# Optimization experiments

Measured on AMD Instinct MI355X. Metric: run time of the kernel, lower is better.

The kernel has to match this reference:

```python
import jax, jax.numpy as jnp
import numpy as np

N, E = 50000, 1_000_000
IN_F, OUT_F = 128, 64
NEG_SLOPE = 0.2


def setup_inputs() -> dict:
    key = jax.random.key(0)
    k1, k2, k3, k4, k5 = jax.random.split(key, 5)
    x = jax.random.normal(k1, (N, IN_F), dtype=jnp.float32)
    edge_index = jax.random.randint(k2, (2, E), 0, N, dtype=jnp.int64)
    # xavier_uniform with gain=1.414 (as in the torch init)
    gain = 1.414
    bW = gain * np.sqrt(6.0 / (IN_F + OUT_F))
    W = jax.random.uniform(k3, (IN_F, OUT_F), jnp.float32, -bW, bW)
    ba = gain * np.sqrt(6.0 / (OUT_F + 1))
    a_src = jax.random.uniform(k4, (OUT_F, 1), jnp.float32, -ba, ba)
    a_dst = jax.random.uniform(k5, (OUT_F, 1), jnp.float32, -ba, ba)
    return {"x": x, "edge_index": edge_index, "W": W, "a_src": a_src, "a_dst": a_dst}


def reference(x, edge_index, W, a_src, a_dst):
    n = x.shape[0]
    Wh = x @ W                                  # [N, F_out]
    src = edge_index[0]
    dst = edge_index[1]
    # per-edge attention logits: (Wh[src] . a_src) + (Wh[dst] . a_dst)
    s_src = Wh @ a_src[:, 0]                    # [N]
    s_dst = Wh @ a_dst[:, 0]                    # [N]
    e = jax.nn.leaky_relu(s_src[src] + s_dst[dst], negative_slope=NEG_SLOPE)  # [E]
    e = jnp.exp(e - jnp.max(e))                 # global-max stabilized exp (matches torch code)
    denom = jax.ops.segment_sum(e, dst, num_segments=n) + 1e-16  # [N]
    alpha = e / denom[dst]                      # [E]  (dropout p=0 -> identity)
    out = jax.ops.segment_sum(Wh[src] * alpha[:, None], dst, num_segments=n)  # [N, F_out]
    return jax.nn.elu(out)
```

## Files before the change

### kernel.cpp

```cpp
#include <hip/hip_runtime.h>
#include <hip/hip_bf16.h>
#include <math.h>

#define NN 50000
#define NE 1000000
#define FIN 128
#define FOUT 64
#define NEG 0.2f

#define NB     1024
#define DPB    50
#define NBUSED 1000
#define TS     4096
#define PADCAP 1280
#define TILE_BLKS 245
#define GEMM_BLKS 391

using short8  = __attribute__((ext_vector_type(8))) short;
using floatx4 = __attribute__((ext_vector_type(4))) float;

static __device__ __forceinline__ short f2bf(float f) {
    __hip_bfloat16 h = __float2bfloat16(f);
    return *(short*)&h;
}

__global__ __launch_bounds__(512) void k_front(
    const float* __restrict__ x, const float* __restrict__ W,
    const float* __restrict__ a_src, const float* __restrict__ a_dst,
    const int* __restrict__ ei,
    __hip_bfloat16* __restrict__ Whb, float* __restrict__ s_src,
    float* __restrict__ s_dst,
    int* __restrict__ bcur, unsigned* __restrict__ bdata2)
{
    __shared__ int cnt[NB];
    __shared__ int ofs[NB];
    __shared__ int cur[NB];
    __shared__ int gpos[NB];
    __shared__ unsigned srt[TS];
    __shared__ int wsum[8];

    const int tid  = threadIdx.x;
    const int lane = tid & 63;
    const int wv   = tid >> 6;

    if (blockIdx.x >= TILE_BLKS) {
        const int col  = lane & 15;
        const int quad = lane >> 4;
        const int strip = (blockIdx.x - TILE_BLKS) * 8 + wv;
        if (strip >= NN / 16) return;
        const int row0 = strip * 16;

        short8 bfr[4][4];
        #pragma unroll
        for (int kk = 0; kk < 4; ++kk) {
            #pragma unroll
            for (int nt = 0; nt < 4; ++nt) {
                const float* wp = W + (kk * 32 + quad * 8) * FOUT + nt * 16 + col;
                #pragma unroll
                for (int j = 0; j < 8; ++j)
                    bfr[kk][nt][j] = f2bf(wp[j * FOUT]);
            }
        }

        floatx4 acc[4] = {{0.f,0.f,0.f,0.f},{0.f,0.f,0.f,0.f},
                          {0.f,0.f,0.f,0.f},{0.f,0.f,0.f,0.f}};

        const float* xrow = x + (size_t)(row0 + col) * FIN + quad * 8;
        #pragma unroll
        for (int kk = 0; kk < 4; ++kk) {
            const float4 u0 = *(const float4*)(xrow + kk * 32);
            const float4 u1 = *(const float4*)(xrow + kk * 32 + 4);
            short8 af;
            af[0] = f2bf(u0.x); af[1] = f2bf(u0.y);
            af[2] = f2bf(u0.z); af[3] = f2bf(u0.w);
            af[4] = f2bf(u1.x); af[5] = f2bf(u1.y);
            af[6] = f2bf(u1.z); af[7] = f2bf(u1.w);
            #pragma unroll
            for (int nt = 0; nt < 4; ++nt)
                acc[nt] = __builtin_amdgcn_mfma_f32_16x16x32_bf16(
                    af, bfr[kk][nt], acc[nt], 0, 0, 0);
        }

        const float av0 = a_src[col], av1 = a_src[16 + col];
        const float av2 = a_src[32 + col], av3 = a_src[48 + col];
        const float bv0 = a_dst[col], bv1 = a_dst[16 + col];
        const float bv2 = a_dst[32 + col], bv3 = a_dst[48 + col];

        float ps[4], pd[4];
        #pragma unroll
        for (int reg = 0; reg < 4; ++reg) {
            ps[reg] = acc[0][reg] * av0 + acc[1][reg] * av1
                    + acc[2][reg] * av2 + acc[3][reg] * av3;
            pd[reg] = acc[0][reg] * bv0 + acc[1][reg] * bv1
                    + acc[2][reg] * bv2 + acc[3][reg] * bv3;
        }

        #pragma unroll
        for (int nt = 0; nt < 4; ++nt)
            #pragma unroll
            for (int reg = 0; reg < 4; ++reg)
                Whb[(size_t)(row0 + quad * 4 + reg) * FOUT + nt * 16 + col] =
                    __float2bfloat16(acc[nt][reg]);

        #pragma unroll
        for (int off = 1; off < 16; off <<= 1) {
            #pragma unroll
            for (int reg = 0; reg < 4; ++reg) {
                ps[reg] += __shfl_xor(ps[reg], off);
                pd[reg] += __shfl_xor(pd[reg], off);
            }
        }
        if (col == 0) {
            #pragma unroll
            for (int reg = 0; reg < 4; ++reg) {
                s_src[row0 + quad * 4 + reg] = ps[reg];
                s_dst[row0 + quad * 4 + reg] = pd[reg];
            }
        }
        return;
    }

    const int tile = blockIdx.x;
    const int base = tile * TS;
    const int tcnt = (NE - base < TS) ? (NE - base) : TS;

    cnt[tid] = 0; cnt[tid + 512] = 0;
    __syncthreads();

    unsigned pk[8];
    #pragma unroll
    for (int j = 0; j < 8; ++j) {
        const int i = j * 512 + tid;
        if (i < tcnt) {
            const int e = base + i;
            const unsigned s = (unsigned)__builtin_nontemporal_load(ei + e);
            const unsigned d = (unsigned)__builtin_nontemporal_load(ei + NE + e);
            pk[j] = (s << 16) | d;
            atomicAdd(&cnt[d / DPB], 1);
        } else pk[j] = 0xFFFFFFFFu;
    }
    __syncthreads();

    {
        const int i0 = tid * 2;
        const int v0 = cnt[i0], v1 = cnt[i0 + 1];
        const int s = v0 + v1;
        int inc = s;
        #pragma unroll
        for (int off = 1; off < 64; off <<= 1) {
            const int t = __shfl_up(inc, off);
            if (lane >= off) inc += t;
        }
        if (lane == 63) wsum[wv] = inc;
        __syncthreads();
        int wb = 0;
        #pragma unroll
        for (int w = 0; w < 7; ++w) if (w < wv) wb += wsum[w];
        const int excl = wb + inc - s;
        ofs[i0]     = excl;      ofs[i0 + 1] = excl + v0;
        cur[i0]     = excl;      cur[i0 + 1] = excl + v0;
        if (v0 > 0) gpos[i0]     = i0 * PADCAP + atomicAdd(&bcur[i0], v0);
        if (v1 > 0) gpos[i0 + 1] = (i0 + 1) * PADCAP + atomicAdd(&bcur[i0 + 1], v1);
    }
    __syncthreads();

    #pragma unroll
    for (int j = 0; j < 8; ++j) {
        if (pk[j] != 0xFFFFFFFFu) {
            const int b = (int)(pk[j] & 0xffffu) / DPB;
            const int pos = atomicAdd(&cur[b], 1);
            srt[pos] = pk[j];
        }
    }
    __syncthreads();

    for (int i = tid; i < tcnt; i += 512) {
        const unsigned p = srt[i];
        const int bb = (int)(p & 0xffffu) / DPB;
        const int dpos = gpos[bb] + (i - ofs[bb]);
        if (dpos < (bb + 1) * PADCAP) bdata2[dpos] = p;
    }
}

__global__ __launch_bounds__(512) void k_sortgather(
    const int* __restrict__ bcur, const unsigned* __restrict__ bdata2,
    const float* __restrict__ s_src, const float* __restrict__ s_dst,
    const __hip_bfloat16* __restrict__ Whb, float* __restrict__ out)
{
    __shared__ unsigned raw[PADCAP];
    __shared__ unsigned srt[PADCAP];
    __shared__ float evs[PADCAP];
    __shared__ float sdl[DPB];
    __shared__ int cnt[64];
    __shared__ int ofs2[65];
    __shared__ int cur[64];

    const int b = blockIdx.x;
    const int tid = threadIdx.x;
    const int lane = tid & 63;
    const int wv = tid >> 6;
    const int d0 = b * DPB;

    if (tid < 64) cnt[tid] = 0;
    if (tid < DPB) sdl[tid] = s_dst[d0 + tid];

    int tot = bcur[b];
    if (tot > PADCAP) tot = PADCAP;
    const unsigned* slab = bdata2 + (size_t)b * PADCAP;

    for (int i = tid; i < tot; i += 512) raw[i] = slab[i];
    __syncthreads();

    for (int i = tid; i < tot; i += 512)
        atomicAdd(&cnt[(int)(raw[i] & 0xffffu) - d0], 1);
    __syncthreads();

    if (tid < 64) {
        const int cc = (tid < DPB) ? cnt[tid] : 0;
        int in2 = cc;
        #pragma unroll
        for (int off = 1; off < 64; off <<= 1) {
            const int t = __shfl_up(in2, off);
            if (tid >= off) in2 += t;
        }
        ofs2[tid + 1] = in2;
        if (tid == 0) ofs2[0] = 0;
        cur[tid] = in2 - cc;
    }
    __syncthreads();

    for (int i = tid; i < tot; i += 512) {
        const unsigned p = raw[i];
        const int j = (int)(p & 0xffffu) - d0;
        const int pos = atomicAdd(&cur[j], 1);
        srt[pos] = p;
        float v = s_src[p >> 16] + sdl[j];
        v = (v > 0.f) ? v : NEG * v;
        evs[pos] = __expf(v);
    }
    __syncthreads();

    for (int j = wv; j < DPB; j += 8) {
        const int d = d0 + j;
        const int beg = ofs2[j];
        const int end = ofs2[j + 1];
        float acc = 0.f, den = 0.f;
        int i = beg;
        for (; i + 8 <= end; i += 8) {
            int ss[8]; float ee[8], w[8];
            #pragma unroll
            for (int k = 0; k < 8; ++k) {
                ss[k] = (int)(srt[i + k] >> 16);
                ee[k] = evs[i + k];
            }
            #pragma unroll
            for (int k = 0; k < 8; ++k)
                w[k] = __bfloat162float(Whb[(size_t)ss[k] * FOUT + lane]);
            #pragma unroll
            for (int k = 0; k < 8; ++k) {
                acc = fmaf(ee[k], w[k], acc);
                den += ee[k];
            }
        }
        for (; i < end; ++i) {
            const int s0 = (int)(srt[i] >> 16);
            const float e0 = evs[i];
            acc = fmaf(e0, __bfloat162float(Whb[(size_t)s0 * FOUT + lane]), acc);
            den += e0;
        }
        const float r = acc / (den + 1e-16f);
        out[(size_t)d * FOUT + lane] = (r > 0.f) ? r : expm1f(r);
    }
}

extern "C" void kernel_launch(void* const* d_in, const int* in_sizes, int n_in,
                              void* d_out, int out_size, void* d_ws, size_t ws_size,
                              hipStream_t stream)
{
    const float* x     = (const float*)d_in[0];
    const int*   ei    = (const int*)d_in[1];
    const float* W     = (const float*)d_in[2];
    const float* a_src = (const float*)d_in[3];
    const float* a_dst = (const float*)d_in[4];
    float* out = (float*)d_out;

    float* ws    = (float*)d_ws;
    __hip_bfloat16* Whb = (__hip_bfloat16*)ws;
    float* s_src = ws + (size_t)NN * FOUT / 2;
    float* s_dst = s_src + NN;
    int*   bcur  = (int*)(s_dst + NN);
    unsigned* bdata2 = (unsigned*)(bcur + NB);

    hipMemsetAsync(bcur, 0, NB * sizeof(int), stream);
    k_front<<<TILE_BLKS + GEMM_BLKS, 512, 0, stream>>>(
        x, W, a_src, a_dst, ei, Whb, s_src, s_dst, bcur, bdata2);
    k_sortgather<<<NBUSED, 512, 0, stream>>>(bcur, bdata2, s_src, s_dst,
                                             Whb, out);
}
```

Baseline: 129.9 us.

## Replace per-destination counting sort with LDS atomic accumulation in gather kernel

The gather kernel no longer counting-sorts edges by destination within each bucket. Each wave takes an even contiguous share of the bucket's edges and atomically adds exp-weighted Wh rows into a shared-memory accumulator, with denominators also summed by atomics. This drops two barriers, the histogram and the scan, and balances load across waves regardless of in-degree skew. In exchange it adds LDS float atomics per edge and lane, which can contend when edges share a destination, and makes the summation order nondeterministic.

After: 453.1 us. 249% more time.

```diff
diff --git a/kernel.cpp b/kernel.cpp
--- a/kernel.cpp
+++ b/kernel.cpp
@@ -182,18 +182,16 @@
     }
 }
 
-__global__ __launch_bounds__(512) void k_sortgather(
+__global__ __launch_bounds__(512) void k_accgather(
     const int* __restrict__ bcur, const unsigned* __restrict__ bdata2,
     const float* __restrict__ s_src, const float* __restrict__ s_dst,
     const __hip_bfloat16* __restrict__ Whb, float* __restrict__ out)
 {
     __shared__ unsigned raw[PADCAP];
-    __shared__ unsigned srt[PADCAP];
     __shared__ float evs[PADCAP];
+    __shared__ float accum[DPB * FOUT];
+    __shared__ float den[DPB];
     __shared__ float sdl[DPB];
-    __shared__ int cnt[64];
-    __shared__ int ofs2[65];
-    __shared__ int cur[64];
 
     const int b = blockIdx.x;
     const int tid = threadIdx.x;
@@ -201,75 +199,55 @@
     const int wv = tid >> 6;
     const int d0 = b * DPB;
 
-    if (tid < 64) cnt[tid] = 0;
-    if (tid < DPB) sdl[tid] = s_dst[d0 + tid];
+    for (int i = tid; i < DPB * FOUT; i += 512) accum[i] = 0.f;
+    if (tid < DPB) { den[tid] = 0.f; sdl[tid] = s_dst[d0 + tid]; }
 
     int tot = bcur[b];
     if (tot > PADCAP) tot = PADCAP;
     const unsigned* slab = bdata2 + (size_t)b * PADCAP;
-
     for (int i = tid; i < tot; i += 512) raw[i] = slab[i];
-    __syncthreads();
-
-    for (int i = tid; i < tot; i += 512)
-        atomicAdd(&cnt[(int)(raw[i] & 0xffffu) - d0], 1);
-    __syncthreads();
-
-    if (tid < 64) {
-        const int cc = (tid < DPB) ? cnt[tid] : 0;
-        int in2 = cc;
-        #pragma unroll
-        for (int off = 1; off < 64; off <<= 1) {
-            const int t = __shfl_up(in2, off);
-            if (tid >= off) in2 += t;
-        }
-        ofs2[tid + 1] = in2;
-        if (tid == 0) ofs2[0] = 0;
-        cur[tid] = in2 - cc;
-    }
     __syncthreads();
 
     for (int i = tid; i < tot; i += 512) {
         const unsigned p = raw[i];
         const int j = (int)(p & 0xffffu) - d0;
-        const int pos = atomicAdd(&cur[j], 1);
-        srt[pos] = p;
         float v = s_src[p >> 16] + sdl[j];
         v = (v > 0.f) ? v : NEG * v;
-        evs[pos] = __expf(v);
+        const float ev = __expf(v);
+        evs[i] = ev;
+        atomicAdd(&den[j], ev);
+    }
+    __syncthreads();
+
+    const int chunk = (tot + 7) >> 3;
+    const int beg = wv * chunk;
+    int end = beg + chunk; if (end > tot) end = tot;
+    int i = beg;
+    for (; i + 4 <= end; i += 4) {
+        const unsigned p0 = raw[i],     p1 = raw[i + 1];
+        const unsigned p2 = raw[i + 2], p3 = raw[i + 3];
+        const float e0 = evs[i],     e1 = evs[i + 1];
+        const float e2 = evs[i + 2], e3 = evs[i + 3];
+        const float w0 = __bfloat162float(Whb[(size_t)(p0 >> 16) * FOUT + lane]);
+        const float w1 = __bfloat162float(Whb[(size_t)(p1 >> 16) * FOUT + lane]);
+        const float w2 = __bfloat162float(Whb[(size_t)(p2 >> 16) * FOUT + lane]);
+        const float w3 = __bfloat162float(Whb[(size_t)(p3 >> 16) * FOUT + lane]);
+        atomicAdd(&accum[((p0 & 0xffffu) - d0) * FOUT + lane], e0 * w0);
+        atomicAdd(&accum[((p1 & 0xffffu) - d0) * FOUT + lane], e1 * w1);
+        atomicAdd(&accum[((p2 & 0xffffu) - d0) * FOUT + lane], e2 * w2);
+        atomicAdd(&accum[((p3 & 0xffffu) - d0) * FOUT + lane], e3 * w3);
+    }
+    for (; i < end; ++i) {
+        const unsigned p0 = raw[i];
+        const float e0 = evs[i];
+        const float w0 = __bfloat162float(Whb[(size_t)(p0 >> 16) * FOUT + lane]);
+        atomicAdd(&accum[((p0 & 0xffffu) - d0) * FOUT + lane], e0 * w0);
     }
     __syncthreads();
 
     for (int j = wv; j < DPB; j += 8) {
-        const int d = d0 + j;
-        const int beg = ofs2[j];
-        const int end = ofs2[j + 1];
-        float acc = 0.f, den = 0.f;
-        int i = beg;
-        for (; i + 8 <= end; i += 8) {
-            int ss[8]; float ee[8], w[8];
-            #pragma unroll
-            for (int k = 0; k < 8; ++k) {
-                ss[k] = (int)(srt[i + k] >> 16);
-                ee[k] = evs[i + k];
-            }
-            #pragma unroll
-            for (int k = 0; k < 8; ++k)
-                w[k] = __bfloat162float(Whb[(size_t)ss[k] * FOUT + lane]);
-            #pragma unroll
-            for (int k = 0; k < 8; ++k) {
-                acc = fmaf(ee[k], w[k], acc);
-                den += ee[k];
-            }
-        }
-        for (; i < end; ++i) {
-            const int s0 = (int)(srt[i] >> 16);
-            const float e0 = evs[i];
-            acc = fmaf(e0, __bfloat162float(Whb[(size_t)s0 * FOUT + lane]), acc);
-            den += e0;
-        }
-        const float r = acc / (den + 1e-16f);
-        out[(size_t)d * FOUT + lane] = (r > 0.f) ? r : expm1f(r);
+        const float r = accum[j * FOUT + lane] / (den[j] + 1e-16f);
+        out[(size_t)(d0 + j) * FOUT + lane] = (r > 0.f) ? r : expm1f(r);
     }
 }
 
@@ -294,6 +272,6 @@
     hipMemsetAsync(bcur, 0, NB * sizeof(int), stream);
     k_front<<<TILE_BLKS + GEMM_BLKS, 512, 0, stream>>>(
         x, W, a_src, a_dst, ei, Whb, s_src, s_dst, bcur, bdata2);
-    k_sortgather<<<NBUSED, 512, 0, stream>>>(bcur, bdata2, s_src, s_dst,
-                                             Whb, out);
-}
+    k_accgather<<<NBUSED, 512, 0, stream>>>(bcur, bdata2, s_src, s_dst,
+                                            Whb, out);
+}
```
